# Kernel optimization log

Hardware: AMD Instinct MI355X
Metric: run time of the kernel (lower is better)

The kernel has to match this reference:

```python
import jax, jax.numpy as jnp
import numpy as np

V, E, H = 32000, 64, 128  # vocab, embed_dim, hidden_dim (from module defaults)
SOS_IDX = 1
PAD_IDX = 0


def lstm_cell(x, h, c, Wih, Whh, b):
    # torch LSTM gate order: input, forget, cell(g), output
    gates = x @ Wih.T + h @ Whh.T + b  # [B, 4H]
    i, f, g, o = jnp.split(gates, 4, axis=-1)
    c = jax.nn.sigmoid(f) * c + jax.nn.sigmoid(i) * jnp.tanh(g)
    h = jax.nn.sigmoid(o) * jnp.tanh(c)
    return h, c


def setup_inputs() -> dict:
    key = jax.random.key(0)
    ks = jax.random.split(key, 11)
    B, T = 32, 128
    s = 1.0 / np.sqrt(H)  # torch default uniform scale ~ 1/sqrt(hidden)
    embed = jax.random.normal(ks[0], (V, E), jnp.float32) * 0.05
    embed = embed.at[PAD_IDX].set(0.0)  # padding_idx row is zeros
    enc_Wih = jax.random.normal(ks[1], (4 * H, E), jnp.float32) * s
    enc_Whh = jax.random.normal(ks[2], (4 * H, H), jnp.float32) * s
    enc_b   = jax.random.normal(ks[3], (4 * H,),  jnp.float32) * s  # b_ih + b_hh fused
    dec_Wih = jax.random.normal(ks[4], (4 * H, E), jnp.float32) * s
    dec_Whh = jax.random.normal(ks[5], (4 * H, H), jnp.float32) * s
    dec_b   = jax.random.normal(ks[6], (4 * H,),  jnp.float32) * s
    fc_w = jax.random.normal(ks[7], (V, H), jnp.float32) * s
    fc_b = jax.random.normal(ks[8], (V,),  jnp.float32) * s
    x = jax.random.randint(ks[9], (B, T), 0, V)
    return dict(x=x, embed=embed, enc_Wih=enc_Wih, enc_Whh=enc_Whh, enc_b=enc_b,
                dec_Wih=dec_Wih, dec_Whh=dec_Whh, dec_b=dec_b, fc_w=fc_w, fc_b=fc_b)


def reference(x, embed, enc_Wih, enc_Whh, enc_b, dec_Wih, dec_Whh, dec_b, fc_w, fc_b):
    B, T = x.shape
    emb = embed[x]  # [B, T, E]
    h0 = jnp.zeros((B, H), emb.dtype)
    c0 = jnp.zeros((B, H), emb.dtype)

    def enc_step(carry, xt):
        h, c = carry
        h, c = lstm_cell(xt, h, c, enc_Wih, enc_Whh, enc_b)
        return (h, c), None

    (h, c), _ = jax.lax.scan(enc_step, (h0, c0), jnp.swapaxes(emb, 0, 1))

    tok0 = jnp.full((B,), SOS_IDX, dtype=jnp.int32)

    def dec_step(carry, _):
        h, c, tok = carry
        e = embed[tok]  # [B, E]
        h, c = lstm_cell(e, h, c, dec_Wih, dec_Whh, dec_b)
        logits = h @ fc_w.T + fc_b  # [B, V]
        tok = jnp.argmax(logits, axis=-1).astype(jnp.int32)  # greedy (target=None path)
        return (h, c, tok), logits

    _, logits = jax.lax.scan(dec_step, (h, c, tok0), None, length=T)
    return jnp.swapaxes(logits, 0, 1)  # [B, T, V]
```

## Files before the change

### kernel.cpp

```cpp
#include <hip/hip_runtime.h>
#include <math.h>

#define BB_ 32
#define TT_ 128
#define EE_ 64
#define HH_ 128
#define VV_ 32000
#define NMM 200
#define NCELL 32
#define NWG (NMM + NCELL)
#define VW 160
#define NSREP 64

#define OFF_LW  0
#define OFF_HSL 81920
#define DYN_LDS 98304
#define OFF_SG  0
#define OFF_SH  2048
#define OFF_TOK 2560
#define OFF_R64 2568

#define WS_HQ    0
#define WS_PART  (TT_*BB_*HH_*4)
#define WS_HSENT (WS_PART + TT_*BB_*NMM*8)
#define WS_ZEND  (WS_HSENT + TT_*NSREP*32*4)
#define WS_HENC  WS_ZEND
#define WS_CENC  (WS_HENC + BB_*HH_*4)
#define WS_END   (WS_CENC + BB_*HH_*4)

__device__ __forceinline__ float rlane(float v, int l){
  return __int_as_float(__builtin_amdgcn_readlane(__float_as_int(v), l));
}
__device__ __forceinline__ float sigm(float x){ return 1.f / (1.f + expf(-x)); }

__device__ __forceinline__ unsigned long long packmax(float v, int idx){
  unsigned u = __float_as_uint(v);
  u = (u & 0x80000000u) ? ~u : (u | 0x80000000u);
  return ((unsigned long long)u << 32) | (unsigned long long)(0xFFFFFFFFu - (unsigned)idx);
}

__device__ __forceinline__ unsigned aload32(const unsigned* p){
  return __hip_atomic_load(p, __ATOMIC_RELAXED, __HIP_MEMORY_SCOPE_AGENT);
}
__device__ __forceinline__ unsigned long long aload64(const unsigned long long* p){
  return __hip_atomic_load(p, __ATOMIC_RELAXED, __HIP_MEMORY_SCOPE_AGENT);
}
__device__ __forceinline__ void astore32(unsigned* p, unsigned v){
  __hip_atomic_store(p, v, __ATOMIC_RELAXED, __HIP_MEMORY_SCOPE_AGENT);
}
__device__ __forceinline__ void astore64(unsigned long long* p, unsigned long long v){
  __hip_atomic_store(p, v, __ATOMIC_RELAXED, __HIP_MEMORY_SCOPE_AGENT);
}

__device__ __forceinline__ float whh_dot(const float* wrow, float h0, float h1){
  const float4* hp = (const float4*)wrow;
  asm volatile("" : "+v"(hp));
  float b0 = 0.f, b1 = 0.f, b2 = 0.f, b3 = 0.f;
#pragma unroll
  for (int q = 0; q < 16; ++q){
    const float4 w = hp[q];
    b0 = fmaf(w.x, rlane(h0, q*4+0), b0);
    b1 = fmaf(w.y, rlane(h0, q*4+1), b1);
    b2 = fmaf(w.z, rlane(h0, q*4+2), b2);
    b3 = fmaf(w.w, rlane(h0, q*4+3), b3);
  }
#pragma unroll
  for (int q = 0; q < 16; ++q){
    const float4 w = hp[16+q];
    b0 = fmaf(w.x, rlane(h1, q*4+0), b0);
    b1 = fmaf(w.y, rlane(h1, q*4+1), b1);
    b2 = fmaf(w.z, rlane(h1, q*4+2), b2);
    b3 = fmaf(w.w, rlane(h1, q*4+3), b3);
  }
  return (b0 + b1) + (b2 + b3);
}

__device__ __forceinline__ float gate_dot_r(const float (&wih)[EE_], const float (&whh)[HH_],
                                            float bias, float xe, float h0, float h1){
  float a0 = bias, a1 = 0.f, a2 = 0.f, a3 = 0.f;
#pragma unroll
  for (int e = 0; e < EE_; e += 4){
    a0 = fmaf(wih[e+0], rlane(xe, e+0), a0);
    a1 = fmaf(wih[e+1], rlane(xe, e+1), a1);
    a2 = fmaf(wih[e+2], rlane(xe, e+2), a2);
    a3 = fmaf(wih[e+3], rlane(xe, e+3), a3);
  }
#pragma unroll
  for (int j = 0; j < 64; j += 4){
    a0 = fmaf(whh[j+0], rlane(h0, j+0), a0);
    a1 = fmaf(whh[j+1], rlane(h0, j+1), a1);
    a2 = fmaf(whh[j+2], rlane(h0, j+2), a2);
    a3 = fmaf(whh[j+3], rlane(h0, j+3), a3);
  }
#pragma unroll
  for (int j = 0; j < 64; j += 4){
    a0 = fmaf(whh[64+j+0], rlane(h1, j+0), a0);
    a1 = fmaf(whh[64+j+1], rlane(h1, j+1), a1);
    a2 = fmaf(whh[64+j+2], rlane(h1, j+2), a2);
    a3 = fmaf(whh[64+j+3], rlane(h1, j+3), a3);
  }
  return (a0 + a1) + (a2 + a3);
}

__global__ __launch_bounds__(512)
void enc_kernel(const int* __restrict__ xt, const float* __restrict__ embed,
                const float* __restrict__ Wih, const float* __restrict__ Whh,
                const float* __restrict__ bv,
                float* __restrict__ h_out, float* __restrict__ c_out)
{
  const int b = blockIdx.x, t = threadIdx.x, lane = t & 63;
  __shared__ float sh[HH_];
  __shared__ float sg[4*HH_];
  float wih[EE_], whh[HH_];
#pragma unroll
  for (int e = 0; e < EE_; ++e) wih[e] = Wih[t*EE_ + e];
#pragma unroll
  for (int j = 0; j < HH_; ++j) whh[j] = Whh[t*HH_ + j];
  const float bias = bv[t];
  float c = 0.f, hv = 0.f;
  if (t < HH_) sh[t] = 0.f;
  __syncthreads();
#pragma unroll 1
  for (int s = 0; s < TT_; ++s){
    const int tok = xt[b*TT_ + s];
    const float xe = embed[tok*EE_ + lane];
    const float h0 = sh[lane], h1 = sh[64 + lane];
    const float g = gate_dot_r(wih, whh, bias, xe, h0, h1);
    __syncthreads();
    sg[t] = g;
    __syncthreads();
    if (t < HH_){
      const float gi = sg[t], gf = sg[128+t], gg = sg[256+t], go = sg[384+t];
      c = sigm(gf)*c + sigm(gi)*tanhf(gg);
      hv = sigm(go)*tanhf(c);
      sh[t] = hv;
    }
    __syncthreads();
  }
  if (t < HH_){ h_out[b*HH_ + t] = hv; c_out[b*HH_ + t] = c; }
}

__global__ __launch_bounds__(512)
void dec_kernel(const float* __restrict__ embed,
                const float* __restrict__ dWih, const float* __restrict__ dWhh,
                const float* __restrict__ db,
                const float* __restrict__ fcw, const float* __restrict__ fcb,
                const float* __restrict__ h_enc, const float* __restrict__ c_enc,
                float* __restrict__ hq, unsigned long long* __restrict__ part,
                unsigned* __restrict__ hsent, float* __restrict__ out)
{
  extern __shared__ char smem[];
  const int t = threadIdx.x;
  const int wg = blockIdx.x;

  if (wg < NCELL){
    float* sg = (float*)(smem + OFF_SG);
    float* sh = (float*)(smem + OFF_SH);
    int* stok = (int*)(smem + OFF_TOK);
    unsigned long long* r64 = (unsigned long long*)(smem + OFF_R64);
    const int b = wg, lane = t & 63;
    const float bias = db[t];
    float wih[EE_];
#pragma unroll
    for (int e = 0; e < EE_; ++e) wih[e] = dWih[t*EE_ + e];
    float c = 0.f;
    if (t < HH_){ c = c_enc[b*HH_ + t]; sh[t] = h_enc[b*HH_ + t]; }
    int tok = 1;
    __syncthreads();
    float hacc = whh_dot(dWhh + t*HH_, sh[lane], sh[64 + lane]);
#pragma unroll 1
    for (int s = 0; s < TT_; ++s){
      const float xe = embed[tok*EE_ + lane];
      float a0 = bias + hacc, a1 = 0.f, a2 = 0.f, a3 = 0.f;
#pragma unroll
      for (int e = 0; e < EE_; e += 4){
        a0 = fmaf(wih[e+0], rlane(xe, e+0), a0);
        a1 = fmaf(wih[e+1], rlane(xe, e+1), a1);
        a2 = fmaf(wih[e+2], rlane(xe, e+2), a2);
        a3 = fmaf(wih[e+3], rlane(xe, e+3), a3);
      }
      sg[t] = (a0 + a1) + (a2 + a3);
      __syncthreads();
      if (t < HH_){
        const float gi = sg[t], gf = sg[128+t], gg = sg[256+t], go = sg[384+t];
        c = sigm(gf)*c + sigm(gi)*tanhf(gg);
        const float hv = sigm(go)*tanhf(c);
        sh[t] = hv;
        __hip_atomic_store((unsigned*)&hq[(size_t)s*BB_*HH_ + b*HH_ + t],
                           __float_as_uint(hv), __ATOMIC_RELAXED, __HIP_MEMORY_SCOPE_AGENT);
      }
      __syncthreads();
      if (t < NSREP) astore32(&hsent[((size_t)s*NSREP + t)*32 + b], 1u);
      const float hacc_n = whh_dot(dWhh + t*HH_, sh[lane], sh[64 + lane]);
      unsigned long long m = 0ull;
      if (t < NMM){
        const unsigned long long* pp = part + ((size_t)s*BB_ + b)*NMM + t;
        bool pf = false;
        for (;;){
          if (!m) m = aload64(pp);
          if (m && !pf){
            pf = true;
            const unsigned idx = 0xFFFFFFFFu - (unsigned)(m & 0xFFFFFFFFull);
            const float* er = embed + (size_t)idx*EE_;
            const float p0 = er[0], p1 = er[32];
            asm volatile("" :: "v"(p0), "v"(p1));
          }
          if (__all(m != 0)) break;
        }
      }
#pragma unroll
      for (int off = 32; off > 0; off >>= 1){
        const unsigned long long o = __shfl_xor(m, off);
        if (o > m) m = o;
      }
      if ((t & 63) == 0) r64[t >> 6] = m;
      __syncthreads();
      if (t == 0){
        unsigned long long best = r64[0];
#pragma unroll
        for (int w = 1; w < 8; ++w) if (r64[w] > best) best = r64[w];
        *stok = (int)(0xFFFFFFFFu - (unsigned)(best & 0xFFFFFFFFull));
      }
      __syncthreads();
      tok = *stok;
      hacc = hacc_n;
    }
  } else {
    const int widx = wg - NCELL;
    const int v0 = widx * VW;
    float4* lw4 = (float4*)(smem + OFF_LW);
    float*  hsl = (float*)(smem + OFF_HSL);
    const int vg = t & 31;
    const int bh = (t >> 5) & 1;
    const int wv = t >> 6;
    const int lane = t & 63;
    const int lr0 = bh, lr1 = bh + 2;
    float* myslot = hsl + wv*4*HH_;
    for (int i = t; i < VW*HH_; i += 512){
      const int r = i >> 7, k = i & 127;
      ((float*)lw4)[((k >> 2)*VW + r)*4 + (k & 3)] = fcw[(size_t)(v0 + r)*HH_ + k];
    }
    float fb[5];
#pragma unroll
    for (int vi = 0; vi < 5; ++vi) fb[vi] = fcb[v0 + vi*32 + vg];
    __syncthreads();
#pragma unroll 1
    for (int s = 0; s < TT_; ++s){
      {
        const int rep = (widx*8 + wv) & (NSREP - 1);
        const unsigned* line = &hsent[((size_t)s*NSREP + rep)*32];
        unsigned v = 1u;
        int wb = 0;
        if (lane < 4){ v = 0u; wb = 2*wv + (lane & 1) + ((lane >> 1) ? 16 : 0); }
        for (;;){
          if (!v) v = aload32(&line[wb]);
          if (__all(v != 0)) break;
        }
      }
      {
        const int row = lane >> 4;
        const int gb  = 2*wv + (row & 1) + ((row >> 1) ? 16 : 0);
        const float4* src = (const float4*)(hq + (size_t)s*BB_*HH_ + gb*HH_);
        const int c0 = (lane & 15) * 2;
        const float4 va = src[c0], vb = src[c0+1];
        float4* dst = (float4*)(myslot + row*HH_);
        dst[c0] = va; dst[c0+1] = vb;
        asm volatile("s_waitcnt lgkmcnt(0)" ::: "memory");
        __builtin_amdgcn_sched_barrier(0);
      }
      float acc[5][2];
#pragma unroll
      for (int vi = 0; vi < 5; ++vi){ acc[vi][0] = 0.f; acc[vi][1] = 0.f; }
#pragma unroll 4
      for (int kcc = 0; kcc < 32; ++kcc){
        const float4 hb0 = *(const float4*)&myslot[lr0*HH_ + kcc*4];
        const float4 hb1 = *(const float4*)&myslot[lr1*HH_ + kcc*4];
#pragma unroll
        for (int vi = 0; vi < 5; ++vi){
          const float4 w = lw4[kcc*VW + vi*32 + vg];
          acc[vi][0] = fmaf(w.x,hb0.x,fmaf(w.y,hb0.y,fmaf(w.z,hb0.z,fmaf(w.w,hb0.w,acc[vi][0]))));
          acc[vi][1] = fmaf(w.x,hb1.x,fmaf(w.y,hb1.y,fmaf(w.z,hb1.z,fmaf(w.w,hb1.w,acc[vi][1]))));
        }
      }
#pragma unroll
      for (int vi = 0; vi < 5; ++vi){ acc[vi][0] += fb[vi]; acc[vi][1] += fb[vi]; }
      const int b0 = 2*wv + bh, b1 = b0 + 16;
#pragma unroll
      for (int bi = 0; bi < 2; ++bi){
        unsigned long long best = 0ull;
#pragma unroll
        for (int vi = 0; vi < 5; ++vi){
          const unsigned long long pk = packmax(acc[vi][bi], v0 + vi*32 + vg);
          if (pk > best) best = pk;
        }
#pragma unroll
        for (int off = 16; off > 0; off >>= 1){
          const unsigned long long o = __shfl_xor(best, off);
          if (o > best) best = o;
        }
        if (vg == 0)
          astore64(&part[((size_t)s*BB_ + (bi ? b1 : b0))*NMM + widx], best);
      }
      {
        float* orow0 = out + ((size_t)b0*TT_ + s)*(size_t)VV_ + v0;
        float* orow1 = out + ((size_t)b1*TT_ + s)*(size_t)VV_ + v0;
#pragma unroll
        for (int vi = 0; vi < 5; ++vi){
          __builtin_nontemporal_store(acc[vi][0], &orow0[vi*32 + vg]);
          __builtin_nontemporal_store(acc[vi][1], &orow1[vi*32 + vg]);
        }
      }
    }
  }
}

extern "C" void kernel_launch(void* const* d_in, const int* in_sizes, int n_in,
                              void* d_out, int out_size, void* d_ws, size_t ws_size,
                              hipStream_t stream){
  (void)in_sizes; (void)n_in; (void)out_size; (void)ws_size;
  const int*   x     = (const int*)  d_in[0];
  const float* embed = (const float*)d_in[1];
  const float* eWih  = (const float*)d_in[2];
  const float* eWhh  = (const float*)d_in[3];
  const float* eb    = (const float*)d_in[4];
  const float* dWih  = (const float*)d_in[5];
  const float* dWhh  = (const float*)d_in[6];
  const float* db    = (const float*)d_in[7];
  const float* fcw   = (const float*)d_in[8];
  const float* fcb   = (const float*)d_in[9];
  float* out = (float*)d_out;
  char* ws = (char*)d_ws;
  float* hq = (float*)(ws + WS_HQ);
  unsigned long long* part = (unsigned long long*)(ws + WS_PART);
  unsigned* hsent = (unsigned*)(ws + WS_HSENT);
  float* h_enc = (float*)(ws + WS_HENC);
  float* c_enc = (float*)(ws + WS_CENC);

  (void)hipMemsetAsync(ws + WS_PART, 0, WS_ZEND - WS_PART, stream);
  (void)hipFuncSetAttribute((const void*)dec_kernel, hipFuncAttributeMaxDynamicSharedMemorySize, DYN_LDS);

  enc_kernel<<<NCELL, 512, 0, stream>>>(x, embed, eWih, eWhh, eb, h_enc, c_enc);
  dec_kernel<<<NWG, 512, DYN_LDS, stream>>>(embed, dWih, dWhh, db, fcw, fcb,
                                            h_enc, c_enc, hq, part, hsent, out);
}
```

Measured before the change: 1.669 ms.

## Embed readiness flags in h-state payload instead of separate hsent flag array

The cell workgroups now publish each pair of hidden values as one 64-bit atomic store, offset by +2 so the word is never zero. Matmul workgroups poll these data words directly and drop the separate hsent flag poll followed by a data load. This removes one synchronization round-trip per step on the decoder's critical path. In exchange the whole hq buffer must be zeroed each call, and the +2 offset adds a small rounding error to h.

After: 1.618 ms. 3.0% less time.

```diff
diff --git a/kernel.cpp b/kernel.cpp
--- a/kernel.cpp
+++ b/kernel.cpp
@@ -10,7 +10,6 @@
 #define NCELL 32
 #define NWG (NMM + NCELL)
 #define VW 160
-#define NSREP 64
 
 #define OFF_LW  0
 #define OFF_HSL 81920
@@ -21,9 +20,8 @@
 #define OFF_R64 2568
 
 #define WS_HQ    0
-#define WS_PART  (TT_*BB_*HH_*4)
-#define WS_HSENT (WS_PART + TT_*BB_*NMM*8)
-#define WS_ZEND  (WS_HSENT + TT_*NSREP*32*4)
+#define WS_PART  (TT_*BB_*64*8)
+#define WS_ZEND  (WS_PART + (size_t)TT_*BB_*NMM*8)
 #define WS_HENC  WS_ZEND
 #define WS_CENC  (WS_HENC + BB_*HH_*4)
 #define WS_END   (WS_CENC + BB_*HH_*4)
@@ -39,14 +37,8 @@
   return ((unsigned long long)u << 32) | (unsigned long long)(0xFFFFFFFFu - (unsigned)idx);
 }
 
-__device__ __forceinline__ unsigned aload32(const unsigned* p){
-  return __hip_atomic_load(p, __ATOMIC_RELAXED, __HIP_MEMORY_SCOPE_AGENT);
-}
 __device__ __forceinline__ unsigned long long aload64(const unsigned long long* p){
   return __hip_atomic_load(p, __ATOMIC_RELAXED, __HIP_MEMORY_SCOPE_AGENT);
-}
-__device__ __forceinline__ void astore32(unsigned* p, unsigned v){
-  __hip_atomic_store(p, v, __ATOMIC_RELAXED, __HIP_MEMORY_SCOPE_AGENT);
 }
 __device__ __forceinline__ void astore64(unsigned long long* p, unsigned long long v){
   __hip_atomic_store(p, v, __ATOMIC_RELAXED, __HIP_MEMORY_SCOPE_AGENT);
@@ -146,8 +138,8 @@
                 const float* __restrict__ db,
                 const float* __restrict__ fcw, const float* __restrict__ fcb,
                 const float* __restrict__ h_enc, const float* __restrict__ c_enc,
-                float* __restrict__ hq, unsigned long long* __restrict__ part,
-                unsigned* __restrict__ hsent, float* __restrict__ out)
+                unsigned long long* __restrict__ hq, unsigned long long* __restrict__ part,
+                float* __restrict__ out)
 {
   extern __shared__ char smem[];
   const int t = threadIdx.x;
@@ -186,11 +178,14 @@
         c = sigm(gf)*c + sigm(gi)*tanhf(gg);
         const float hv = sigm(go)*tanhf(c);
         sh[t] = hv;
-        __hip_atomic_store((unsigned*)&hq[(size_t)s*BB_*HH_ + b*HH_ + t],
-                           __float_as_uint(hv), __ATOMIC_RELAXED, __HIP_MEMORY_SCOPE_AGENT);
+        const float hp2 = hv + 2.0f;
+        const float pr  = __shfl_xor(hp2, 1);
+        if (!(t & 1))
+          astore64(&hq[(size_t)s*BB_*64 + b*64 + (t >> 1)],
+                   (unsigned long long)__float_as_uint(hp2) |
+                   ((unsigned long long)__float_as_uint(pr) << 32));
       }
       __syncthreads();
-      if (t < NSREP) astore32(&hsent[((size_t)s*NSREP + t)*32 + b], 1u);
       const float hacc_n = whh_dot(dWhh + t*HH_, sh[lane], sh[64 + lane]);
       unsigned long long m = 0ull;
       if (t < NMM){
@@ -247,24 +242,25 @@
 #pragma unroll 1
     for (int s = 0; s < TT_; ++s){
       {
-        const int rep = (widx*8 + wv) & (NSREP - 1);
-        const unsigned* line = &hsent[((size_t)s*NSREP + rep)*32];
-        unsigned v = 1u;
-        int wb = 0;
-        if (lane < 4){ v = 0u; wb = 2*wv + (lane & 1) + ((lane >> 1) ? 16 : 0); }
-        for (;;){
-          if (!v) v = aload32(&line[wb]);
-          if (__all(v != 0)) break;
-        }
-      }
-      {
         const int row = lane >> 4;
         const int gb  = 2*wv + (row & 1) + ((row >> 1) ? 16 : 0);
-        const float4* src = (const float4*)(hq + (size_t)s*BB_*HH_ + gb*HH_);
-        const int c0 = (lane & 15) * 2;
-        const float4 va = src[c0], vb = src[c0+1];
-        float4* dst = (float4*)(myslot + row*HH_);
-        dst[c0] = va; dst[c0+1] = vb;
+        const unsigned long long* pp = hq + (size_t)s*BB_*64 + gb*64 + (lane & 15)*4;
+        unsigned long long g0 = 0, g1 = 0, g2 = 0, g3 = 0;
+        for (;;){
+          if (!g0) g0 = aload64(pp + 0);
+          if (!g1) g1 = aload64(pp + 1);
+          if (!g2) g2 = aload64(pp + 2);
+          if (!g3) g3 = aload64(pp + 3);
+          if (__all(g0 && g1 && g2 && g3)) break;
+        }
+        float2 f0, f1, f2, f3;
+        f0.x = __uint_as_float((unsigned)g0) - 2.0f; f0.y = __uint_as_float((unsigned)(g0>>32)) - 2.0f;
+        f1.x = __uint_as_float((unsigned)g1) - 2.0f; f1.y = __uint_as_float((unsigned)(g1>>32)) - 2.0f;
+        f2.x = __uint_as_float((unsigned)g2) - 2.0f; f2.y = __uint_as_float((unsigned)(g2>>32)) - 2.0f;
+        f3.x = __uint_as_float((unsigned)g3) - 2.0f; f3.y = __uint_as_float((unsigned)(g3>>32)) - 2.0f;
+        float* dst = myslot + row*HH_ + (lane & 15)*8;
+        *(float2*)(dst+0) = f0; *(float2*)(dst+2) = f1;
+        *(float2*)(dst+4) = f2; *(float2*)(dst+6) = f3;
         asm volatile("s_waitcnt lgkmcnt(0)" ::: "memory");
         __builtin_amdgcn_sched_barrier(0);
       }
@@ -330,16 +326,15 @@
   const float* fcb   = (const float*)d_in[9];
   float* out = (float*)d_out;
   char* ws = (char*)d_ws;
-  float* hq = (float*)(ws + WS_HQ);
+  unsigned long long* hq   = (unsigned long long*)(ws + WS_HQ);
   unsigned long long* part = (unsigned long long*)(ws + WS_PART);
-  unsigned* hsent = (unsigned*)(ws + WS_HSENT);
   float* h_enc = (float*)(ws + WS_HENC);
   float* c_enc = (float*)(ws + WS_CENC);
 
-  (void)hipMemsetAsync(ws + WS_PART, 0, WS_ZEND - WS_PART, stream);
+  (void)hipMemsetAsync(ws, 0, WS_ZEND, stream);
   (void)hipFuncSetAttribute((const void*)dec_kernel, hipFuncAttributeMaxDynamicSharedMemorySize, DYN_LDS);
 
   enc_kernel<<<NCELL, 512, 0, stream>>>(x, embed, eWih, eWhh, eb, h_enc, c_enc);
   dec_kernel<<<NWG, 512, DYN_LDS, stream>>>(embed, dWih, dWhh, db, fcw, fcb,
-                                            h_enc, c_enc, hq, part, hsent, out);
-}
+                                            h_enc, c_enc, hq, part, out);
+}
```
